# Performance work log

Measured on AMD Instinct MI355X. Metric: run time of the kernel, lower is better.

## Reference

```python
import jax, jax.numpy as jnp
import numpy as np

N, M, D = 8192, 8192, 128

def setup_inputs() -> dict:
    key = jax.random.key(0)
    kq, kk, kv = jax.random.split(key, 3)
    Q = jax.random.normal(kq, (N, D), dtype=jnp.float32)
    K = jax.random.normal(kk, (M, D), dtype=jnp.float32)
    V = jax.random.normal(kv, (M, D), dtype=jnp.float32)
    return {"Q": Q, "K": K, "V": V}

def reference(Q, K, V):
    # scores: [N, M], unscaled QK^T
    scores = Q @ K.T
    # NOTE: original uses torch.softmax(scores, dim=0, dtype=float) -> softmax over the
    # QUERY axis (axis 0), normalizing each key-column across queries.
    attn = jax.nn.softmax(scores.astype(jnp.float32), axis=0)
    return attn @ V  # [N, D]
```

## Files before the change

### kernel.cpp

```cpp
#include <hip/hip_runtime.h>
#include <hip/hip_bf16.h>
#include <math.h>

constexpr int N = 8192, M = 8192, D = 128;
constexpr int NE = N * D;
constexpr float SHIFT = 60.0f;
constexpr int SN_A = 16;
constexpr int PC_KS = 16;
constexpr int MK = M / 32;

typedef unsigned short u16;
using short8 = __attribute__((ext_vector_type(8))) short;
using f32x4  = __attribute__((ext_vector_type(4))) float;

#define MFMA16(a, b, c) __builtin_amdgcn_mfma_f32_16x16x32_bf16((a), (b), (c), 0, 0, 0)

constexpr int PR = 40;
constexpr int KP = 136;
constexpr int WP = 72;
constexpr int PP = 72;

__device__ __forceinline__ u16 f2bf_rn(float x) {
  unsigned int u = __float_as_uint(x);
  return (u16)((u + 0x7fffu + ((u >> 16) & 1u)) >> 16);
}
__device__ __forceinline__ float bf2f(u16 h) { return __uint_as_float((unsigned)h << 16); }

__device__ __forceinline__ size_t qk_frag(int rowblk, int kblk, int lane) {
  return (((size_t)rowblk * 4 + kblk) * 64 + lane) * 8;
}
__device__ __forceinline__ size_t pw_frag(int blk16, int mkblk, int lane) {
  return (((size_t)blk16 * MK + mkblk) * 64 + lane) * 8;
}

__global__ __launch_bounds__(256) void convert_frag(const float4* __restrict__ Qs,
                                                    const float4* __restrict__ Ks,
                                                    u16* __restrict__ Qhi, u16* __restrict__ Qlo,
                                                    u16* __restrict__ Khi, u16* __restrict__ Klo) {
  int idx = blockIdx.x * 256 + threadIdx.x;
  int n = idx >> 4, g = idx & 15;
  const float4* src = blockIdx.y ? Ks : Qs;
  u16* hi = blockIdx.y ? Khi : Qhi;
  u16* lo = blockIdx.y ? Klo : Qlo;
  float4 f0 = src[n * 32 + g * 2], f1 = src[n * 32 + g * 2 + 1];
  float v[8] = {f0.x, f0.y, f0.z, f0.w, f1.x, f1.y, f1.z, f1.w};
  short8 hs, ls;
#pragma unroll
  for (int j = 0; j < 8; ++j) {
    u16 h = f2bf_rn(v[j]);
    hs[j] = (short)h;
    ls[j] = (short)f2bf_rn(v[j] - bf2f(h));
  }
  size_t off = qk_frag(n >> 4, g >> 2, (n & 15) + ((g & 3) << 4));
  *(short8*)(hi + off) = hs;
  *(short8*)(lo + off) = ls;
}

__global__ __launch_bounds__(256, 4) void pass_a_frag(const u16* __restrict__ Qh,
                                                      const u16* __restrict__ Ql,
                                                      const u16* __restrict__ Kh,
                                                      const u16* __restrict__ Kl,
                                                      float* __restrict__ colsum,
                                                      u16* __restrict__ Pf) {
  __shared__ u16 PW[4][32 * PR];
  const int tid = threadIdx.x;
  const int w = tid >> 6, lane = tid & 63;
  const int r = lane & 15, q = lane >> 4;
  const int cbase = blockIdx.x * 128 + 32 * w;
  const int mymk = blockIdx.x * 4 + w;
  const int n0 = blockIdx.y * (N / SN_A);
  u16* pw = PW[w];

  short8 kh[4][2], kl[4][2];
#pragma unroll
  for (int kk = 0; kk < 4; ++kk)
#pragma unroll
    for (int c = 0; c < 2; ++c) {
      size_t off = qk_frag((cbase >> 4) + c, kk, lane);
      kh[kk][c] = *(const short8*)(Kh + off);
      kl[kk][c] = *(const short8*)(Kl + off);
    }

  float csum[2] = {0.f, 0.f};

  for (int s = 0; s < 16; ++s) {
    const int nb = n0 + s * 32;

    f32x4 acc[2][2];
#pragma unroll
    for (int t = 0; t < 2; ++t)
#pragma unroll
      for (int c = 0; c < 2; ++c) acc[t][c] = (f32x4){0.f, 0.f, 0.f, 0.f};

#pragma unroll
    for (int kk = 0; kk < 4; ++kk) {
      short8 ah[2], al[2];
#pragma unroll
      for (int t = 0; t < 2; ++t) {
        size_t off = qk_frag((nb >> 4) + t, kk, lane);
        ah[t] = *(const short8*)(Qh + off);
        al[t] = *(const short8*)(Ql + off);
      }
#pragma unroll
      for (int t = 0; t < 2; ++t)
#pragma unroll
        for (int c = 0; c < 2; ++c) {
          acc[t][c] = MFMA16(ah[t], kh[kk][c], acc[t][c]);
          acc[t][c] = MFMA16(al[t], kh[kk][c], acc[t][c]);
          acc[t][c] = MFMA16(ah[t], kl[kk][c], acc[t][c]);
        }
    }

#pragma unroll
    for (int t = 0; t < 2; ++t)
#pragma unroll
      for (int c = 0; c < 2; ++c)
#pragma unroll
        for (int rg = 0; rg < 4; ++rg) {
          float e = __expf(acc[t][c][rg] - SHIFT);
          csum[c] += e;
          pw[(16 * t + 4 * q + rg) * PR + 16 * c + r] = f2bf_rn(e);
        }
#pragma unroll
    for (int t = 0; t < 2; ++t) {
      short8 v = *(const short8*)(pw + (16 * t + r) * PR + q * 8);
      *(short8*)(Pf + pw_frag((nb >> 4) + t, mymk, lane)) = v;
    }
  }

  csum[0] += __shfl_xor(csum[0], 16);
  csum[0] += __shfl_xor(csum[0], 32);
  csum[1] += __shfl_xor(csum[1], 16);
  csum[1] += __shfl_xor(csum[1], 32);
  if (lane < 16) {
    atomicAdd(&colsum[cbase + r], csum[0]);
    atomicAdd(&colsum[cbase + 16 + r], csum[1]);
  }
}

__global__ __launch_bounds__(256) void scale_transpose_frag(const float* __restrict__ V,
                                                            const float* __restrict__ colsum,
                                                            u16* __restrict__ Wf) {
  __shared__ float Vs[64][132];
  __shared__ float rls[64];
  const int tid = threadIdx.x;
  const int m0 = blockIdx.x * 64;
#pragma unroll
  for (int it = 0; it < 8; ++it) {
    int idx = tid + it * 256;
    int rr = idx >> 5, g = idx & 31;
    float4 v = *(const float4*)(V + (size_t)(m0 + rr) * D + g * 4);
    Vs[rr][g * 4 + 0] = v.x; Vs[rr][g * 4 + 1] = v.y;
    Vs[rr][g * 4 + 2] = v.z; Vs[rr][g * 4 + 3] = v.w;
  }
  if (tid < 64) rls[tid] = 1.0f / colsum[m0 + tid];
  __syncthreads();
#pragma unroll
  for (int it = 0; it < 4; ++it) {
    int idx = tid + it * 256;
    int dd = idx >> 3, g = idx & 7;
    short8 o;
#pragma unroll
    for (int j = 0; j < 8; ++j) {
      int mm = g * 8 + j;
      o[j] = (short)f2bf_rn(Vs[mm][dd] * rls[mm]);
    }
    *(short8*)(Wf + pw_frag(dd >> 4, (m0 >> 5) + (g >> 2), (dd & 15) + ((g & 3) << 4))) = o;
  }
}

template <bool ATOMIC>
__global__ __launch_bounds__(256, 4) void pass_c_kern(const u16* __restrict__ Pf,
                                                      const u16* __restrict__ Wf,
                                                      float* __restrict__ dst) {
  const int tid = threadIdx.x;
  const int w = tid >> 6, lane = tid & 63;
  const int r = lane & 15, q = lane >> 4;
  const int nblk0 = blockIdx.x * 8 + w * 2;
  const int mk0 = blockIdx.y * (MK / PC_KS);

  f32x4 acc[2][8];
#pragma unroll
  for (int i = 0; i < 2; ++i)
#pragma unroll
    for (int dt = 0; dt < 8; ++dt) acc[i][dt] = (f32x4){0.f, 0.f, 0.f, 0.f};

  short8 a0 = *(const short8*)(Pf + pw_frag(nblk0 + 0, mk0, lane));
  short8 a1 = *(const short8*)(Pf + pw_frag(nblk0 + 1, mk0, lane));

  for (int mk = 0; mk < MK / PC_KS; ++mk) {
    const int mkg = mk0 + mk;
    const int mkn = mk + 1 < MK / PC_KS ? mkg + 1 : mk0;
    short8 a0n = *(const short8*)(Pf + pw_frag(nblk0 + 0, mkn, lane));
    short8 a1n = *(const short8*)(Pf + pw_frag(nblk0 + 1, mkn, lane));
#pragma unroll
    for (int dt = 0; dt < 8; ++dt) {
      short8 b = *(const short8*)(Wf + pw_frag(dt, mkg, lane));
      acc[0][dt] = MFMA16(a0, b, acc[0][dt]);
      acc[1][dt] = MFMA16(a1, b, acc[1][dt]);
    }
    a0 = a0n;
    a1 = a1n;
  }

  if (ATOMIC) {
#pragma unroll
    for (int i = 0; i < 2; ++i)
#pragma unroll
      for (int dt = 0; dt < 8; ++dt)
#pragma unroll
        for (int rg = 0; rg < 4; ++rg)
          atomicAdd(&dst[(size_t)((nblk0 + i) * 16 + q * 4 + rg) * D + dt * 16 + r],
                    acc[i][dt][rg]);
  } else {
    float* part = dst + (size_t)blockIdx.y * NE;
#pragma unroll
    for (int i = 0; i < 2; ++i)
#pragma unroll
      for (int dt = 0; dt < 8; ++dt)
#pragma unroll
        for (int rg = 0; rg < 4; ++rg)
          part[(size_t)((nblk0 + i) * 16 + q * 4 + rg) * D + dt * 16 + r] = acc[i][dt][rg];
  }
}

__global__ __launch_bounds__(256) void reduce_out(const float4* __restrict__ part,
                                                  float4* __restrict__ out) {
  int i = blockIdx.x * 256 + threadIdx.x;
  float4 s = part[i];
#pragma unroll
  for (int k = 1; k < PC_KS; ++k) {
    float4 p = part[(size_t)k * (NE / 4) + i];
    s.x += p.x; s.y += p.y; s.z += p.z; s.w += p.w;
  }
  out[i] = s;
}

__global__ __launch_bounds__(256) void convert_hilo2(const float4* __restrict__ Qs,
                                                     const float4* __restrict__ Ks,
                                                     ushort4* __restrict__ Qhi, ushort4* __restrict__ Qlo,
                                                     ushort4* __restrict__ Khi, ushort4* __restrict__ Klo) {
  int i = blockIdx.x * 256 + threadIdx.x;
  const float4* src = blockIdx.y ? Ks : Qs;
  ushort4* hi = blockIdx.y ? Khi : Qhi;
  ushort4* lo = blockIdx.y ? Klo : Qlo;
  float4 f = src[i];
  float v[4] = {f.x, f.y, f.z, f.w};
  u16 hs[4], ls[4];
#pragma unroll
  for (int j = 0; j < 4; ++j) {
    hs[j] = f2bf_rn(v[j]);
    ls[j] = f2bf_rn(v[j] - bf2f(hs[j]));
  }
  hi[i] = make_ushort4(hs[0], hs[1], hs[2], hs[3]);
  lo[i] = make_ushort4(ls[0], ls[1], ls[2], ls[3]);
}

__global__ __launch_bounds__(256, 4) void pass_a_fb(const u16* __restrict__ Qh,
                                                    const u16* __restrict__ Ql,
                                                    const u16* __restrict__ Kh,
                                                    const u16* __restrict__ Kl,
                                                    float* __restrict__ colsum) {
  const int tid = threadIdx.x;
  const int w = tid >> 6, lane = tid & 63;
  const int r = lane & 15, q = lane >> 4;
  const int cbase = blockIdx.x * 128 + 32 * w;
  const int n0 = blockIdx.y * (N / SN_A);

  short8 kh[4][2], kl[4][2];
#pragma unroll
  for (int kk = 0; kk < 4; ++kk)
#pragma unroll
    for (int c = 0; c < 2; ++c) {
      kh[kk][c] = *(const short8*)(Kh + (size_t)(cbase + 16 * c + r) * D + kk * 32 + q * 8);
      kl[kk][c] = *(const short8*)(Kl + (size_t)(cbase + 16 * c + r) * D + kk * 32 + q * 8);
    }

  float csum[2] = {0.f, 0.f};
  for (int s = 0; s < 16; ++s) {
    const int nb = n0 + s * 32;
    f32x4 acc[2][2];
#pragma unroll
    for (int t = 0; t < 2; ++t)
#pragma unroll
      for (int c = 0; c < 2; ++c) acc[t][c] = (f32x4){0.f, 0.f, 0.f, 0.f};
#pragma unroll
    for (int kk = 0; kk < 4; ++kk) {
      short8 ah[2], al[2];
#pragma unroll
      for (int t = 0; t < 2; ++t) {
        ah[t] = *(const short8*)(Qh + (size_t)(nb + t * 16 + r) * D + kk * 32 + q * 8);
        al[t] = *(const short8*)(Ql + (size_t)(nb + t * 16 + r) * D + kk * 32 + q * 8);
      }
#pragma unroll
      for (int t = 0; t < 2; ++t)
#pragma unroll
        for (int c = 0; c < 2; ++c) {
          acc[t][c] = MFMA16(ah[t], kh[kk][c], acc[t][c]);
          acc[t][c] = MFMA16(al[t], kh[kk][c], acc[t][c]);
          acc[t][c] = MFMA16(ah[t], kl[kk][c], acc[t][c]);
        }
    }
#pragma unroll
    for (int t = 0; t < 2; ++t)
#pragma unroll
      for (int c = 0; c < 2; ++c)
#pragma unroll
        for (int rg = 0; rg < 4; ++rg) csum[c] += __expf(acc[t][c][rg] - SHIFT);
  }
  csum[0] += __shfl_xor(csum[0], 16);
  csum[0] += __shfl_xor(csum[0], 32);
  csum[1] += __shfl_xor(csum[1], 16);
  csum[1] += __shfl_xor(csum[1], 32);
  if (lane < 16) {
    atomicAdd(&colsum[cbase + r], csum[0]);
    atomicAdd(&colsum[cbase + 16 + r], csum[1]);
  }
}

__global__ __launch_bounds__(256) void scale_transpose_fb(const float* __restrict__ V,
                                                          const float* __restrict__ colsum,
                                                          u16* __restrict__ Wt) {
  __shared__ float Vs[64][132];
  __shared__ float rls[64];
  const int tid = threadIdx.x;
  const int m0 = blockIdx.x * 64;
#pragma unroll
  for (int it = 0; it < 8; ++it) {
    int idx = tid + it * 256;
    int rr = idx >> 5, g = idx & 31;
    float4 v = *(const float4*)(V + (size_t)(m0 + rr) * D + g * 4);
    Vs[rr][g * 4 + 0] = v.x; Vs[rr][g * 4 + 1] = v.y;
    Vs[rr][g * 4 + 2] = v.z; Vs[rr][g * 4 + 3] = v.w;
  }
  if (tid < 64) rls[tid] = 1.0f / colsum[m0 + tid];
  __syncthreads();
#pragma unroll
  for (int it = 0; it < 4; ++it) {
    int idx = tid + it * 256;
    int dd = idx >> 3, g = idx & 7;
    short8 o;
#pragma unroll
    for (int j = 0; j < 8; ++j) {
      int mm = g * 8 + j;
      o[j] = (short)f2bf_rn(Vs[mm][dd] * rls[mm]);
    }
    *(short8*)(Wt + (size_t)dd * M + m0 + g * 8) = o;
  }
}

__global__ __launch_bounds__(256, 2) void pass_c_fb(const u16* __restrict__ Qh,
                                                    const u16* __restrict__ Ql,
                                                    const u16* __restrict__ Kh,
                                                    const u16* __restrict__ Kl,
                                                    const u16* __restrict__ Wt,
                                                    float* __restrict__ out) {
  __shared__ u16 KsH[64 * KP];
  __shared__ u16 KsL[64 * KP];
  __shared__ u16 Ws[128 * WP];
  __shared__ u16 Ps[4][16 * PP];
  const int tid = threadIdx.x;
  const int w = tid >> 6, lane = tid & 63;
  const int r = lane & 15, q = lane >> 4;
  const size_t nrow = (size_t)blockIdx.x * 64 + w * 16 + r;
  const int mbase = blockIdx.y * (M / 4);

  short8 qh[4], ql[4];
#pragma unroll
  for (int kk = 0; kk < 4; ++kk) {
    qh[kk] = *(const short8*)(Qh + nrow * D + kk * 32 + q * 8);
    ql[kk] = *(const short8*)(Ql + nrow * D + kk * 32 + q * 8);
  }

  f32x4 oacc[8];
#pragma unroll
  for (int dt = 0; dt < 8; ++dt) oacc[dt] = (f32x4){0.f, 0.f, 0.f, 0.f};

  for (int mt = 0; mt < (M / 4) / 64; ++mt) {
    const int m0 = mbase + mt * 64;
    __syncthreads();
#pragma unroll
    for (int it = 0; it < 4; ++it) {
      int idx = tid + it * 256;
      int rr = idx >> 4, g = idx & 15;
      *(short8*)(KsH + rr * KP + g * 8) = *(const short8*)(Kh + (size_t)(m0 + rr) * D + g * 8);
      *(short8*)(KsL + rr * KP + g * 8) = *(const short8*)(Kl + (size_t)(m0 + rr) * D + g * 8);
    }
#pragma unroll
    for (int it = 0; it < 4; ++it) {
      int idx = tid + it * 256;
      int dd = idx >> 3, g = idx & 7;
      *(short8*)(Ws + dd * WP + g * 8) = *(const short8*)(Wt + (size_t)dd * M + m0 + g * 8);
    }
    __syncthreads();

    f32x4 sacc[4];
#pragma unroll
    for (int t = 0; t < 4; ++t) sacc[t] = (f32x4){0.f, 0.f, 0.f, 0.f};
#pragma unroll
    for (int kk = 0; kk < 4; ++kk) {
      short8 bh[4], bl[4];
#pragma unroll
      for (int t = 0; t < 4; ++t) {
        bh[t] = *(const short8*)(KsH + (t * 16 + r) * KP + kk * 32 + q * 8);
        bl[t] = *(const short8*)(KsL + (t * 16 + r) * KP + kk * 32 + q * 8);
      }
#pragma unroll
      for (int t = 0; t < 4; ++t) {
        sacc[t] = MFMA16(qh[kk], bh[t], sacc[t]);
        sacc[t] = MFMA16(qh[kk], bl[t], sacc[t]);
        sacc[t] = MFMA16(ql[kk], bh[t], sacc[t]);
      }
    }
#pragma unroll
    for (int t = 0; t < 4; ++t)
#pragma unroll
      for (int rg = 0; rg < 4; ++rg)
        Ps[w][(q * 4 + rg) * PP + t * 16 + r] = f2bf_rn(__expf(sacc[t][rg] - SHIFT));
#pragma unroll
    for (int kk = 0; kk < 2; ++kk) {
      short8 pa = *(const short8*)(Ps[w] + r * PP + kk * 32 + q * 8);
#pragma unroll
      for (int dt = 0; dt < 8; ++dt) {
        short8 wb = *(const short8*)(Ws + (dt * 16 + r) * WP + kk * 32 + q * 8);
        oacc[dt] = MFMA16(pa, wb, oacc[dt]);
      }
    }
  }
#pragma unroll
  for (int dt = 0; dt < 8; ++dt)
#pragma unroll
    for (int rg = 0; rg < 4; ++rg)
      atomicAdd(&out[((size_t)blockIdx.x * 64 + w * 16 + q * 4 + rg) * D + dt * 16 + r],
                oacc[dt][rg]);
}

extern "C" void kernel_launch(void* const* d_in, const int* in_sizes, int n_in,
                              void* d_out, int out_size, void* d_ws, size_t ws_size,
                              hipStream_t stream) {
  const float* Q = (const float*)d_in[0];
  const float* K = (const float*)d_in[1];
  const float* V = (const float*)d_in[2];
  float* out = (float*)d_out;

  u16* Qh = (u16*)d_ws;
  u16* Ql = Qh + NE;
  u16* Kh = Ql + NE;
  u16* Kl = Kh + NE;
  u16* Wb = Kl + NE;
  float* colsum = (float*)(Wb + NE);
  u16* Pf = (u16*)(colsum + M);
  float* Opart = (float*)(Pf + (size_t)N * M);
  const size_t need_mat = (size_t)5 * NE * 2 + M * 4 + (size_t)N * M * 2;
  const size_t need_part = need_mat + (size_t)PC_KS * NE * 4;
  const bool mat = ws_size >= need_mat;
  const bool part = ws_size >= need_part;

  hipMemsetAsync(colsum, 0, M * sizeof(float), stream);
  if (!part) hipMemsetAsync(d_out, 0, (size_t)N * D * sizeof(float), stream);

  if (mat) {
    convert_frag<<<dim3(N * 16 / 256, 2), 256, 0, stream>>>(
        (const float4*)Q, (const float4*)K, Qh, Ql, Kh, Kl);
    pass_a_frag<<<dim3(M / 128, SN_A), 256, 0, stream>>>(Qh, Ql, Kh, Kl, colsum, Pf);
    scale_transpose_frag<<<M / 64, 256, 0, stream>>>(V, colsum, Wb);
    if (part) {
      pass_c_kern<false><<<dim3(N / 128, PC_KS), 256, 0, stream>>>(Pf, Wb, Opart);
      reduce_out<<<NE / 4 / 256, 256, 0, stream>>>((const float4*)Opart, (float4*)out);
    } else {
      pass_c_kern<true><<<dim3(N / 128, PC_KS), 256, 0, stream>>>(Pf, Wb, out);
    }
  } else {
    convert_hilo2<<<dim3(NE / 4 / 256, 2), 256, 0, stream>>>(
        (const float4*)Q, (const float4*)K, (ushort4*)Qh, (ushort4*)Ql, (ushort4*)Kh, (ushort4*)Kl);
    pass_a_fb<<<dim3(M / 128, SN_A), 256, 0, stream>>>(Qh, Ql, Kh, Kl, colsum);
    scale_transpose_fb<<<M / 64, 256, 0, stream>>>(V, colsum, Wb);
    pass_c_fb<<<dim3(N / 64, 4), 256, 0, stream>>>(Qh, Ql, Kh, Kl, Wb, out);
  }
}
```

Baseline: 174.7 us.

## Fold log2e into Q, use exp2 with bias-initialized accumulators, repack K columns

Q is pre-scaled by log2(e) during conversion, so pass A can use a native exp2 with the shift folded into the accumulator's initial value instead of subtracting and calling expf. The K fragments are reordered so each lane holds two adjacent columns, which lets P be written to shared memory as packed 32-bit pairs and changes the colsum indexing to match. Pass A now splits the query axis into twice as many blocks with a higher occupancy hint, and pass C prefetches two K-steps ahead instead of one. The risks are extra rounding from scaling Q before the hi/lo split, and greater register pressure in pass C.

```diff
diff --git a/kernel.cpp b/kernel.cpp
--- a/kernel.cpp
+++ b/kernel.cpp
@@ -5,15 +5,24 @@
 constexpr int N = 8192, M = 8192, D = 128;
 constexpr int NE = N * D;
 constexpr float SHIFT = 60.0f;
-constexpr int SN_A = 16;
+constexpr float LOG2E = 1.4426950408889634f;
+constexpr float S2 = 86.56170245333781f;
+constexpr int SN_A = 32;
 constexpr int PC_KS = 16;
 constexpr int MK = M / 32;
 
 typedef unsigned short u16;
+typedef unsigned int u32;
 using short8 = __attribute__((ext_vector_type(8))) short;
 using f32x4  = __attribute__((ext_vector_type(4))) float;
 
 #define MFMA16(a, b, c) __builtin_amdgcn_mfma_f32_16x16x32_bf16((a), (b), (c), 0, 0, 0)
+
+#if __has_builtin(__builtin_amdgcn_exp2f)
+#define EXP2(x) __builtin_amdgcn_exp2f(x)
+#else
+#define EXP2(x) __expf((x) * 0.6931471805599453f)
+#endif
 
 constexpr int PR = 40;
 constexpr int KP = 136;
@@ -39,24 +48,33 @@
                                                     u16* __restrict__ Khi, u16* __restrict__ Klo) {
   int idx = blockIdx.x * 256 + threadIdx.x;
   int n = idx >> 4, g = idx & 15;
-  const float4* src = blockIdx.y ? Ks : Qs;
-  u16* hi = blockIdx.y ? Khi : Qhi;
-  u16* lo = blockIdx.y ? Klo : Qlo;
+  const bool isK = blockIdx.y != 0;
+  const float4* src = isK ? Ks : Qs;
+  u16* hi = isK ? Khi : Qhi;
+  u16* lo = isK ? Klo : Qlo;
+  const float sc = isK ? 1.0f : LOG2E;
   float4 f0 = src[n * 32 + g * 2], f1 = src[n * 32 + g * 2 + 1];
   float v[8] = {f0.x, f0.y, f0.z, f0.w, f1.x, f1.y, f1.z, f1.w};
   short8 hs, ls;
 #pragma unroll
   for (int j = 0; j < 8; ++j) {
-    u16 h = f2bf_rn(v[j]);
+    float x = v[j] * sc;
+    u16 h = f2bf_rn(x);
     hs[j] = (short)h;
-    ls[j] = (short)f2bf_rn(v[j] - bf2f(h));
-  }
-  size_t off = qk_frag(n >> 4, g >> 2, (n & 15) + ((g & 3) << 4));
+    ls[j] = (short)f2bf_rn(x - bf2f(h));
+  }
+  size_t off;
+  if (isK) {
+    int c = n & 1, r = (n & 31) >> 1;
+    off = qk_frag((n >> 5) * 2 + c, g >> 2, r + ((g & 3) << 4));
+  } else {
+    off = qk_frag(n >> 4, g >> 2, (n & 15) + ((g & 3) << 4));
+  }
   *(short8*)(hi + off) = hs;
   *(short8*)(lo + off) = ls;
 }
 
-__global__ __launch_bounds__(256, 4) void pass_a_frag(const u16* __restrict__ Qh,
+__global__ __launch_bounds__(256, 6) void pass_a_frag(const u16* __restrict__ Qh,
                                                       const u16* __restrict__ Ql,
                                                       const u16* __restrict__ Kh,
                                                       const u16* __restrict__ Kl,
@@ -70,6 +88,7 @@
   const int mymk = blockIdx.x * 4 + w;
   const int n0 = blockIdx.y * (N / SN_A);
   u16* pw = PW[w];
+  u32* pwD = (u32*)pw;
 
   short8 kh[4][2], kl[4][2];
 #pragma unroll
@@ -83,14 +102,14 @@
 
   float csum[2] = {0.f, 0.f};
 
-  for (int s = 0; s < 16; ++s) {
+  for (int s = 0; s < (N / SN_A) / 32; ++s) {
     const int nb = n0 + s * 32;
 
     f32x4 acc[2][2];
 #pragma unroll
     for (int t = 0; t < 2; ++t)
 #pragma unroll
-      for (int c = 0; c < 2; ++c) acc[t][c] = (f32x4){0.f, 0.f, 0.f, 0.f};
+      for (int c = 0; c < 2; ++c) acc[t][c] = (f32x4){-S2, -S2, -S2, -S2};
 
 #pragma unroll
     for (int kk = 0; kk < 4; ++kk) {
@@ -114,13 +133,14 @@
 #pragma unroll
     for (int t = 0; t < 2; ++t)
 #pragma unroll
-      for (int c = 0; c < 2; ++c)
-#pragma unroll
-        for (int rg = 0; rg < 4; ++rg) {
-          float e = __expf(acc[t][c][rg] - SHIFT);
-          csum[c] += e;
-          pw[(16 * t + 4 * q + rg) * PR + 16 * c + r] = f2bf_rn(e);
-        }
+      for (int rg = 0; rg < 4; ++rg) {
+        float e0 = EXP2(acc[t][0][rg]);
+        float e1 = EXP2(acc[t][1][rg]);
+        csum[0] += e0;
+        csum[1] += e1;
+        u32 pk = (u32)f2bf_rn(e0) | ((u32)f2bf_rn(e1) << 16);
+        pwD[(16 * t + 4 * q + rg) * (PR / 2) + r] = pk;
+      }
 #pragma unroll
     for (int t = 0; t < 2; ++t) {
       short8 v = *(const short8*)(pw + (16 * t + r) * PR + q * 8);
@@ -133,8 +153,8 @@
   csum[1] += __shfl_xor(csum[1], 16);
   csum[1] += __shfl_xor(csum[1], 32);
   if (lane < 16) {
-    atomicAdd(&colsum[cbase + r], csum[0]);
-    atomicAdd(&colsum[cbase + 16 + r], csum[1]);
+    atomicAdd(&colsum[cbase + 2 * lane], csum[0]);
+    atomicAdd(&colsum[cbase + 2 * lane + 1], csum[1]);
   }
 }
 
@@ -178,6 +198,7 @@
   const int r = lane & 15, q = lane >> 4;
   const int nblk0 = blockIdx.x * 8 + w * 2;
   const int mk0 = blockIdx.y * (MK / PC_KS);
+  constexpr int CNT = MK / PC_KS;
 
   f32x4 acc[2][8];
 #pragma unroll
@@ -185,22 +206,23 @@
 #pragma unroll
     for (int dt = 0; dt < 8; ++dt) acc[i][dt] = (f32x4){0.f, 0.f, 0.f, 0.f};
 
-  short8 a0 = *(const short8*)(Pf + pw_frag(nblk0 + 0, mk0, lane));
-  short8 a1 = *(const short8*)(Pf + pw_frag(nblk0 + 1, mk0, lane));
-
-  for (int mk = 0; mk < MK / PC_KS; ++mk) {
+  short8 c0 = *(const short8*)(Pf + pw_frag(nblk0 + 0, mk0, lane));
+  short8 c1 = *(const short8*)(Pf + pw_frag(nblk0 + 1, mk0, lane));
+  short8 x0 = *(const short8*)(Pf + pw_frag(nblk0 + 0, mk0 + 1, lane));
+  short8 x1 = *(const short8*)(Pf + pw_frag(nblk0 + 1, mk0 + 1, lane));
+
+  for (int mk = 0; mk < CNT; ++mk) {
     const int mkg = mk0 + mk;
-    const int mkn = mk + 1 < MK / PC_KS ? mkg + 1 : mk0;
-    short8 a0n = *(const short8*)(Pf + pw_frag(nblk0 + 0, mkn, lane));
-    short8 a1n = *(const short8*)(Pf + pw_frag(nblk0 + 1, mkn, lane));
+    const int mk2 = mk + 2 < CNT ? mkg + 2 : mk0;
+    short8 p0 = *(const short8*)(Pf + pw_frag(nblk0 + 0, mk2, lane));
+    short8 p1 = *(const short8*)(Pf + pw_frag(nblk0 + 1, mk2, lane));
 #pragma unroll
     for (int dt = 0; dt < 8; ++dt) {
       short8 b = *(const short8*)(Wf + pw_frag(dt, mkg, lane));
-      acc[0][dt] = MFMA16(a0, b, acc[0][dt]);
-      acc[1][dt] = MFMA16(a1, b, acc[1][dt]);
-    }
-    a0 = a0n;
-    a1 = a1n;
+      acc[0][dt] = MFMA16(c0, b, acc[0][dt]);
+      acc[1][dt] = MFMA16(c1, b, acc[1][dt]);
+    }
+    c0 = x0; c1 = x1; x0 = p0; x1 = p1;
   }
 
   if (ATOMIC) {
@@ -265,7 +287,7 @@
   const int w = tid >> 6, lane = tid & 63;
   const int r = lane & 15, q = lane >> 4;
   const int cbase = blockIdx.x * 128 + 32 * w;
-  const int n0 = blockIdx.y * (N / SN_A);
+  const int n0 = blockIdx.y * (N / 16);
 
   short8 kh[4][2], kl[4][2];
 #pragma unroll
@@ -473,7 +495,7 @@
   } else {
     convert_hilo2<<<dim3(NE / 4 / 256, 2), 256, 0, stream>>>(
         (const float4*)Q, (const float4*)K, (ushort4*)Qh, (ushort4*)Ql, (ushort4*)Kh, (ushort4*)Kl);
-    pass_a_fb<<<dim3(M / 128, SN_A), 256, 0, stream>>>(Qh, Ql, Kh, Kl, colsum);
+    pass_a_fb<<<dim3(M / 128, 16), 256, 0, stream>>>(Qh, Ql, Kh, Kl, colsum);
     scale_transpose_fb<<<M / 64, 256, 0, stream>>>(V, colsum, Wb);
     pass_c_fb<<<dim3(N / 64, 4), 256, 0, stream>>>(Qh, Ql, Kh, Kl, Wb, out);
   }
```

After: 256.1 us. 1.47x slower.
